# Performance work log

Measured on AMD Instinct MI355X. Metric: run time of the kernel, lower is better.

Reference implementation:

```python
import jax, jax.numpy as jnp
import numpy as np

# Qwen2 MoE MLP layer: top-k router -> token dispatch -> grouped SwiGLU MLP -> weighted combine.
S, B, H = 2048, 1, 1024      # seq, batch, hidden
E, K, F = 8, 2, 1408         # num_experts, top_k, moe_intermediate (fc1 emits 2*F for SwiGLU)

def setup_inputs() -> dict:
    key = jax.random.key(0)
    k1, k2, k3, k4 = jax.random.split(key, 4)
    return {
        "hidden_states": jax.random.normal(k1, (S, B, H), jnp.float32),
        "router_weight": jax.random.normal(k2, (H, E), jnp.float32) * 0.02,
        "w1": jax.random.normal(k3, (E, H, 2 * F), jnp.float32) * 0.02,  # grouped fc1 (gate|up)
        "w2": jax.random.normal(k4, (E, F, H), jnp.float32) * 0.02,      # grouped fc2
    }

def reference(hidden_states, router_weight, w1, w2):
    s, b, h = hidden_states.shape
    x = hidden_states.reshape(-1, h)                      # [T, H], T = S*B
    logits = x @ router_weight                            # [T, E]
    probs = jax.nn.softmax(logits, axis=-1)
    _, topk_idx = jax.lax.top_k(probs, K)                 # token -> top-k expert ids
    routing_map = jax.nn.one_hot(topk_idx, E, dtype=probs.dtype).sum(axis=1)  # [T, E] 0/1 mask
    local_probs = probs * routing_map                     # combine weights, zero off-topk
    # Grouped SwiGLU MLP. The torch module permutes tokens to expert groups and runs
    # grouped GEMMs; with static shapes the equivalent math is dense-per-expert with
    # the routing mask folded into the combine weights (identical output).
    y = jnp.einsum('th,ehf->tef', x, w1)                  # [T, E, 2F]
    y1, y2 = jnp.split(y, 2, axis=-1)
    g = jax.nn.silu(y1) * y2                              # swiglu, [T, E, F]
    o = jnp.einsum('tef,efh->teh', g, w2)                 # [T, E, H]
    out = jnp.einsum('teh,te->th', o, local_probs)        # unpermute + prob-weighted combine
    return out.reshape(s, b, h)
```

## Files before the change

### kernel.cpp

```cpp
#include <hip/hip_runtime.h>
#include <hip/hip_bf16.h>
#include <stdint.h>

#define T_TOK 2048
#define HD    1024
#define NE    8
#define FD    1408
#define F2D   2816

#define BM 128
#define BK 32
#define MAXMT 40
#define MAXSLOTS 5120
#define FC1_NT 22
#define FC2_NT 16
#define FC1_NWG (FC1_NT * MAXMT)
#define FC2_NWG (FC2_NT * MAXMT)
#define FC1_CHUNK 110
#define FC2_CHUNK 80

typedef __attribute__((ext_vector_type(8))) short bf16x8;
typedef __attribute__((ext_vector_type(4))) float f32x4;

__device__ __forceinline__ unsigned short f2bf(float f) {
  unsigned int u = __float_as_uint(f);
  u += 0x7FFFu + ((u >> 16) & 1u);
  return (unsigned short)(u >> 16);
}

#define GLL16(gp, lp) __builtin_amdgcn_global_load_lds( \
    (const __attribute__((address_space(1))) void*)(gp), \
    (__attribute__((address_space(3))) void*)(lp), 16, 0, 0)

__global__ __launch_bounds__(256) void k_router(
    const float* __restrict__ x, const float* __restrict__ rw,
    unsigned short* __restrict__ xbf, int* __restrict__ ctrl,
    int* __restrict__ tok_e, float* __restrict__ tok_p)
{
  const int lane = threadIdx.x & 63;
  const int t = blockIdx.x * 4 + (threadIdx.x >> 6);
  const float* xr = x + (size_t)t * HD;

  float part[8];
#pragma unroll
  for (int e = 0; e < 8; ++e) part[e] = 0.f;

#pragma unroll
  for (int i = 0; i < 16; ++i) {
    const int h = i * 64 + lane;
    const float xv = xr[h];
    xbf[(size_t)t * HD + h] = f2bf(xv);
    const float4* rwr = reinterpret_cast<const float4*>(rw + (size_t)h * 8);
    float4 a = rwr[0], b = rwr[1];
    part[0] += xv * a.x; part[1] += xv * a.y; part[2] += xv * a.z; part[3] += xv * a.w;
    part[4] += xv * b.x; part[5] += xv * b.y; part[6] += xv * b.z; part[7] += xv * b.w;
  }
#pragma unroll
  for (int e = 0; e < 8; ++e) {
    float v = part[e];
#pragma unroll
    for (int d = 32; d; d >>= 1) v += __shfl_xor(v, d, 64);
    part[e] = v;
  }
  float m = part[0];
#pragma unroll
  for (int e = 1; e < 8; ++e) m = fmaxf(m, part[e]);
  float p[8], s = 0.f;
#pragma unroll
  for (int e = 0; e < 8; ++e) { p[e] = __expf(part[e] - m); s += p[e]; }
  const float inv = 1.f / s;
#pragma unroll
  for (int e = 0; e < 8; ++e) p[e] *= inv;

  int e0 = 0; float p0 = p[0];
#pragma unroll
  for (int e = 1; e < 8; ++e) if (p[e] > p0) { p0 = p[e]; e0 = e; }
  int e1 = -1; float p1 = -1.f;
#pragma unroll
  for (int e = 0; e < 8; ++e) if (e != e0 && p[e] > p1) { p1 = p[e]; e1 = e; }

  if (lane == 0) {
    tok_e[t * 2 + 0] = e0; tok_e[t * 2 + 1] = e1;
    tok_p[t * 2 + 0] = p0; tok_p[t * 2 + 1] = p1;
    atomicAdd(&ctrl[e0], 1);
    atomicAdd(&ctrl[e1], 1);
  }
}

__global__ __launch_bounds__(256) void k_offsets(
    int* __restrict__ ctrl, int* __restrict__ stok, float* __restrict__ sp,
    int* __restrict__ widmt1, int* __restrict__ widmt2)
{
  __shared__ int soff[8], scnt[8], sFirst[8], sNmt[8], sTake[8];
  __shared__ int sSpill;
  if (threadIdx.x == 0) {
    int o = 0, nm = 0, spill = 0;
    for (int e = 0; e < 8; ++e) {
      ctrl[16 + e] = o; soff[e] = o; scnt[e] = ctrl[e];
      const int n = ctrl[e];
      const int nmt = (n + BM - 1) / BM;
      sFirst[e] = nm; sNmt[e] = nmt; sTake[e] = nmt < 5 ? nmt : 5;
      if (nmt > 5) spill = 1;
      for (int j = 0; j < nmt; ++j) { ctrl[24 + nm] = e; ctrl[64 + nm] = o + j * BM; ++nm; }
      o += nmt * BM;
    }
    for (int i = nm; i < MAXMT; ++i) ctrl[24 + i] = -1;
    sSpill = spill;
  }
  __syncthreads();
  for (int i = threadIdx.x; i < FC1_NWG; i += 256) {
    const int e = i / FC1_CHUNK, r = i % FC1_CHUNK;
    const int j = r / FC1_NT, n = r % FC1_NT;
    widmt1[i] = (j < sTake[e]) ? (sFirst[e] + j) * 32 + n : -1;
  }
  for (int i = threadIdx.x; i < FC2_NWG; i += 256) {
    const int e = i / FC2_CHUNK, r = i % FC2_CHUNK;
    const int j = r / FC2_NT, n = r % FC2_NT;
    widmt2[i] = (j < sTake[e]) ? (sFirst[e] + j) * 32 + n : -1;
  }
  __syncthreads();
  if (sSpill && threadIdx.x == 0) {
    int cur = 0;
    for (int e = 0; e < 8; ++e)
      for (int j = 5; j < sNmt[e]; ++j)
        for (int n = 0; n < FC1_NT; ++n) {
          while (widmt1[cur] != -1) ++cur;
          widmt1[cur] = (sFirst[e] + j) * 32 + n;
        }
    cur = 0;
    for (int e = 0; e < 8; ++e)
      for (int j = 5; j < sNmt[e]; ++j)
        for (int n = 0; n < FC2_NT; ++n) {
          while (widmt2[cur] != -1) ++cur;
          widmt2[cur] = (sFirst[e] + j) * 32 + n;
        }
  }
  for (int e = 0; e < 8; ++e) {
    const int n = scnt[e], o = soff[e];
    const int padEnd = (n + BM - 1) / BM * BM;
    for (int j = n + (int)threadIdx.x; j < padEnd; j += 256) {
      stok[o + j] = 0; sp[o + j] = 0.f;
    }
  }
}

__global__ __launch_bounds__(256) void k_scatter(
    int* __restrict__ ctrl, const int* __restrict__ tok_e,
    const float* __restrict__ tok_p, int* __restrict__ stok,
    float* __restrict__ sp, int* __restrict__ tslot)
{
  const int t = blockIdx.x * 256 + threadIdx.x;
#pragma unroll
  for (int k = 0; k < 2; ++k) {
    const int e = tok_e[t * 2 + k];
    const float pp = tok_p[t * 2 + k];
    const int pos = atomicAdd(&ctrl[8 + e], 1);
    const int slot = ctrl[16 + e] + pos;
    stok[slot] = t; sp[slot] = pp;
    tslot[t * 2 + k] = slot;
  }
}

__global__ __launch_bounds__(256) void k_transpose_cvt(
    const float* __restrict__ src, unsigned short* __restrict__ dst,
    int R, int C)
{
  const size_t zoff = (size_t)blockIdx.z * R * C;
  src += zoff; dst += zoff;
  const int r0 = blockIdx.y * 64, c0 = blockIdx.x * 64;
  __shared__ float tile[64][65];
  const int tr = threadIdx.x >> 4;
  const int tc = (threadIdx.x & 15) * 4;
#pragma unroll
  for (int p = 0; p < 4; ++p) {
    const int r = p * 16 + tr;
    float4 v = *reinterpret_cast<const float4*>(&src[(size_t)(r0 + r) * C + c0 + tc]);
    tile[r][tc + 0] = v.x; tile[r][tc + 1] = v.y;
    tile[r][tc + 2] = v.z; tile[r][tc + 3] = v.w;
  }
  __syncthreads();
#pragma unroll
  for (int p = 0; p < 4; ++p) {
    const int c = p * 16 + tr;
    ushort4 o;
    o.x = f2bf(tile[tc + 0][c]);
    o.y = f2bf(tile[tc + 1][c]);
    o.z = f2bf(tile[tc + 2][c]);
    o.w = f2bf(tile[tc + 3][c]);
    *reinterpret_cast<ushort4*>(&dst[(size_t)(c0 + c) * R + r0 + tc]) = o;
  }
}

__global__ __launch_bounds__(256) void k_fc1(
    const unsigned short* __restrict__ xbf,
    const unsigned short* __restrict__ w1t,
    const int* __restrict__ ctrl,
    const int* __restrict__ stok,
    const float* __restrict__ sp,
    const int* __restrict__ widmt1,
    unsigned short* __restrict__ g)
{
  const int bid = blockIdx.x;
  const int wid = (bid & 7) * FC1_CHUNK + (bid >> 3);
  const int packed = widmt1[wid];
  if (packed < 0) return;
  const int mt = packed >> 5;
  const int e = ctrl[24 + mt];
  const int rowbase = ctrl[64 + mt];
  const int n0 = (packed & 31) * 64;

  __shared__ unsigned short sA[3][BM * BK];
  __shared__ unsigned short sB1[3][64 * BK];
  __shared__ unsigned short sB2[3][64 * BK];

  const int tid = threadIdx.x;
  const int lane = tid & 63;
  const int wave = tid >> 6;
  const int wm = wave >> 1, wn = wave & 1;

  const int schunk = (lane & 3) ^ ((lane >> 3) & 3);
  const unsigned short* aSrc[2];
#pragma unroll
  for (int t4 = 0; t4 < 2; ++t4) {
    const int row = (t4 * 4 + wave) * 16 + (lane >> 2);
    const int tok = stok[rowbase + row];
    aSrc[t4] = xbf + (size_t)tok * HD + schunk * 8;
  }
  const int brow = wave * 16 + (lane >> 2);
  const unsigned short* b1Src = w1t + ((size_t)e * F2D + n0 + brow) * HD + schunk * 8;
  const unsigned short* b2Src = w1t + ((size_t)e * F2D + FD + n0 + brow) * HD + schunk * 8;

  const int c = lane >> 4;
  int aoff[4], boff[2];
#pragma unroll
  for (int m = 0; m < 4; ++m) {
    const int row = wm * 64 + m * 16 + (lane & 15);
    aoff[m] = row * 32 + ((c ^ ((row >> 1) & 3)) << 3);
  }
#pragma unroll
  for (int n = 0; n < 2; ++n) {
    const int row = wn * 32 + n * 16 + (lane & 15);
    boff[n] = row * 32 + ((c ^ ((row >> 1) & 3)) << 3);
  }

  const f32x4 zero = {0.f, 0.f, 0.f, 0.f};
  f32x4 acc1[4][2], acc2[4][2];
#pragma unroll
  for (int m = 0; m < 4; ++m)
#pragma unroll
    for (int n = 0; n < 2; ++n) { acc1[m][n] = zero; acc2[m][n] = zero; }

  auto STAGE = [&](int buf, int k0) {
#pragma unroll
    for (int t4 = 0; t4 < 2; ++t4)
      GLL16(aSrc[t4] + k0, &sA[buf][(t4 * 4 + wave) * 512]);
    GLL16(b1Src + k0, &sB1[buf][wave * 512]);
    GLL16(b2Src + k0, &sB2[buf][wave * 512]);
  };

  const int NSTEP = HD / BK;
  STAGE(0, 0);
  STAGE(1, BK);
  int bsel = 0;
  for (int t = 0; t < NSTEP; ++t) {
    if (t < NSTEP - 2) { asm volatile("s_waitcnt vmcnt(4)" ::: "memory"); }
    else               { asm volatile("s_waitcnt vmcnt(0)" ::: "memory"); }
    __builtin_amdgcn_s_barrier();
    __builtin_amdgcn_sched_barrier(0);
    if (t + 2 < NSTEP) {
      int bnext = bsel + 2; if (bnext >= 3) bnext -= 3;
      STAGE(bnext, (t + 2) * BK);
    }
    bf16x8 af[4], b1f[2], b2f[2];
#pragma unroll
    for (int m = 0; m < 4; ++m)
      af[m] = *(const bf16x8*)&sA[bsel][aoff[m]];
#pragma unroll
    for (int n = 0; n < 2; ++n) {
      b1f[n] = *(const bf16x8*)&sB1[bsel][boff[n]];
      b2f[n] = *(const bf16x8*)&sB2[bsel][boff[n]];
    }
    asm volatile("s_waitcnt lgkmcnt(0)" ::: "memory");
    __builtin_amdgcn_sched_barrier(0);
    __builtin_amdgcn_s_setprio(1);
#pragma unroll
    for (int m = 0; m < 4; ++m)
#pragma unroll
      for (int n = 0; n < 2; ++n) {
        acc1[m][n] = __builtin_amdgcn_mfma_f32_16x16x32_bf16(af[m], b1f[n], acc1[m][n], 0, 0, 0);
        acc2[m][n] = __builtin_amdgcn_mfma_f32_16x16x32_bf16(af[m], b2f[n], acc2[m][n], 0, 0, 0);
      }
    __builtin_amdgcn_s_setprio(0);
    bsel = bsel + 1 == 3 ? 0 : bsel + 1;
  }

  float prv[4][4];
#pragma unroll
  for (int m = 0; m < 4; ++m)
#pragma unroll
    for (int r = 0; r < 4; ++r)
      prv[m][r] = sp[rowbase + wm * 64 + m * 16 + (lane >> 4) * 4 + r];

#pragma unroll
  for (int m = 0; m < 4; ++m) {
    const int rb = rowbase + wm * 64 + m * 16 + (lane >> 4) * 4;
#pragma unroll
    for (int n = 0; n < 2; ++n) {
      const int col = n0 + wn * 32 + n * 16 + (lane & 15);
#pragma unroll
      for (int r = 0; r < 4; ++r) {
        const float y1 = acc1[m][n][r];
        const float y2 = acc2[m][n][r];
        const float gv = y1 / (1.f + __expf(-y1)) * y2 * prv[m][r];
        g[(size_t)(rb + r) * FD + col] = f2bf(gv);
      }
    }
  }
}

__global__ __launch_bounds__(256) void k_fc2(
    const unsigned short* __restrict__ g,
    const unsigned short* __restrict__ w2t,
    const int* __restrict__ ctrl,
    const int* __restrict__ widmt2,
    float* __restrict__ o)
{
  const int bid = blockIdx.x;
  const int wid = (bid & 7) * FC2_CHUNK + (bid >> 3);
  const int packed = widmt2[wid];
  if (packed < 0) return;
  const int mt = packed >> 5;
  const int e = ctrl[24 + mt];
  const int rowbase = ctrl[64 + mt];
  const int n0 = (packed & 31) * 64;

  __shared__ unsigned short sA[3][BM * BK];
  __shared__ unsigned short sB[3][64 * BK];

  const int tid = threadIdx.x;
  const int lane = tid & 63;
  const int wave = tid >> 6;
  const int wm = wave >> 1, wn = wave & 1;

  const int schunk = (lane & 3) ^ ((lane >> 3) & 3);
  const unsigned short* aSrc[2];
#pragma unroll
  for (int t4 = 0; t4 < 2; ++t4) {
    const int row = (t4 * 4 + wave) * 16 + (lane >> 2);
    aSrc[t4] = g + (size_t)(rowbase + row) * FD + schunk * 8;
  }
  const int brow = wave * 16 + (lane >> 2);
  const unsigned short* bSrc = w2t + ((size_t)e * HD + n0 + brow) * FD + schunk * 8;

  const int c = lane >> 4;
  int aoff[4], boff[2];
#pragma unroll
  for (int m = 0; m < 4; ++m) {
    const int row = wm * 64 + m * 16 + (lane & 15);
    aoff[m] = row * 32 + ((c ^ ((row >> 1) & 3)) << 3);
  }
#pragma unroll
  for (int n = 0; n < 2; ++n) {
    const int row = wn * 32 + n * 16 + (lane & 15);
    boff[n] = row * 32 + ((c ^ ((row >> 1) & 3)) << 3);
  }

  const f32x4 zero = {0.f, 0.f, 0.f, 0.f};
  f32x4 acc[4][2];
#pragma unroll
  for (int m = 0; m < 4; ++m)
#pragma unroll
    for (int n = 0; n < 2; ++n) acc[m][n] = zero;

  auto STAGE = [&](int buf, int k0) {
#pragma unroll
    for (int t4 = 0; t4 < 2; ++t4)
      GLL16(aSrc[t4] + k0, &sA[buf][(t4 * 4 + wave) * 512]);
    GLL16(bSrc + k0, &sB[buf][wave * 512]);
  };

  const int NSTEP = FD / BK;
  STAGE(0, 0);
  STAGE(1, BK);
  int bsel = 0;
  for (int t = 0; t < NSTEP; ++t) {
    if (t < NSTEP - 2) { asm volatile("s_waitcnt vmcnt(3)" ::: "memory"); }
    else               { asm volatile("s_waitcnt vmcnt(0)" ::: "memory"); }
    __builtin_amdgcn_s_barrier();
    __builtin_amdgcn_sched_barrier(0);
    if (t + 2 < NSTEP) {
      int bnext = bsel + 2; if (bnext >= 3) bnext -= 3;
      STAGE(bnext, (t + 2) * BK);
    }
    bf16x8 af[4], bf[2];
#pragma unroll
    for (int m = 0; m < 4; ++m)
      af[m] = *(const bf16x8*)&sA[bsel][aoff[m]];
#pragma unroll
    for (int n = 0; n < 2; ++n)
      bf[n] = *(const bf16x8*)&sB[bsel][boff[n]];
    asm volatile("s_waitcnt lgkmcnt(0)" ::: "memory");
    __builtin_amdgcn_sched_barrier(0);
    __builtin_amdgcn_s_setprio(1);
#pragma unroll
    for (int m = 0; m < 4; ++m)
#pragma unroll
      for (int n = 0; n < 2; ++n)
        acc[m][n] = __builtin_amdgcn_mfma_f32_16x16x32_bf16(af[m], bf[n], acc[m][n], 0, 0, 0);
    __builtin_amdgcn_s_setprio(0);
    bsel = bsel + 1 == 3 ? 0 : bsel + 1;
  }

#pragma unroll
  for (int m = 0; m < 4; ++m) {
    const int rb = rowbase + wm * 64 + m * 16 + (lane >> 4) * 4;
#pragma unroll
    for (int n = 0; n < 2; ++n) {
      const int col = n0 + wn * 32 + n * 16 + (lane & 15);
#pragma unroll
      for (int r = 0; r < 4; ++r)
        o[(size_t)(rb + r) * HD + col] = acc[m][n][r];
    }
  }
}

__global__ __launch_bounds__(256) void k_combine(
    const float* __restrict__ o, const int* __restrict__ tslot,
    float* __restrict__ out)
{
  const int t = blockIdx.x;
  const int c4 = threadIdx.x;
  const int sA = tslot[t * 2], sB = tslot[t * 2 + 1];
  const float4 a = reinterpret_cast<const float4*>(o)[(size_t)sA * 256 + c4];
  const float4 b = reinterpret_cast<const float4*>(o)[(size_t)sB * 256 + c4];
  float4 r;
  r.x = a.x + b.x; r.y = a.y + b.y; r.z = a.z + b.z; r.w = a.w + b.w;
  reinterpret_cast<float4*>(out)[(size_t)t * 256 + c4] = r;
}

extern "C" void kernel_launch(void* const* d_in, const int* in_sizes, int n_in,
                              void* d_out, int out_size, void* d_ws, size_t ws_size,
                              hipStream_t stream)
{
  const float* x  = (const float*)d_in[0];
  const float* rw = (const float*)d_in[1];
  const float* w1 = (const float*)d_in[2];
  const float* w2 = (const float*)d_in[3];
  float* out = (float*)d_out;
  char* ws = (char*)d_ws;

  int*   ctrl   = (int*)(ws + 0);
  int*   tok_e  = (int*)(ws + 1024);
  float* tok_p  = (float*)(ws + 17408);
  int*   stok   = (int*)(ws + 33792);
  float* sp     = (float*)(ws + 54272);
  int*   tslot  = (int*)(ws + 74752);
  int*   widmt1 = (int*)(ws + 91136);
  int*   widmt2 = (int*)(ws + 94656);
  unsigned short* xbf = (unsigned short*)(ws + 97280);
  unsigned short* w1t = (unsigned short*)(ws + 4291584);
  unsigned short* w2t = (unsigned short*)(ws + 50428928);
  unsigned short* g   = (unsigned short*)(ws + 73497600);
  float* o = (float*)(ws + 4291584);

  hipMemsetAsync(ws, 0, 1024, stream);

  k_router<<<T_TOK / 4, 256, 0, stream>>>(x, rw, xbf, ctrl, tok_e, tok_p);
  k_transpose_cvt<<<dim3(F2D / 64, HD / 64, NE), 256, 0, stream>>>(w1, w1t, HD, F2D);
  k_transpose_cvt<<<dim3(HD / 64, FD / 64, NE), 256, 0, stream>>>(w2, w2t, FD, HD);
  k_offsets<<<1, 256, 0, stream>>>(ctrl, stok, sp, widmt1, widmt2);
  k_scatter<<<T_TOK / 256, 256, 0, stream>>>(ctrl, tok_e, tok_p, stok, sp, tslot);
  k_fc1<<<FC1_NWG, 256, 0, stream>>>(xbf, w1t, ctrl, stok, sp, widmt1, g);
  k_fc2<<<FC2_NWG, 256, 0, stream>>>(g, w2t, ctrl, widmt2, o);
  k_combine<<<T_TOK, 256, 0, stream>>>(o, tslot, out);
}
```

Baseline: 208.2 us.

## Fuse weight transpose and bf16 conversion into expert GEMM B-tile loads

```diff
diff --git a/kernel.cpp b/kernel.cpp
--- a/kernel.cpp
+++ b/kernel.cpp
@@ -161,39 +161,9 @@
   }
 }
 
-__global__ __launch_bounds__(256) void k_transpose_cvt(
-    const float* __restrict__ src, unsigned short* __restrict__ dst,
-    int R, int C)
-{
-  const size_t zoff = (size_t)blockIdx.z * R * C;
-  src += zoff; dst += zoff;
-  const int r0 = blockIdx.y * 64, c0 = blockIdx.x * 64;
-  __shared__ float tile[64][65];
-  const int tr = threadIdx.x >> 4;
-  const int tc = (threadIdx.x & 15) * 4;
-#pragma unroll
-  for (int p = 0; p < 4; ++p) {
-    const int r = p * 16 + tr;
-    float4 v = *reinterpret_cast<const float4*>(&src[(size_t)(r0 + r) * C + c0 + tc]);
-    tile[r][tc + 0] = v.x; tile[r][tc + 1] = v.y;
-    tile[r][tc + 2] = v.z; tile[r][tc + 3] = v.w;
-  }
-  __syncthreads();
-#pragma unroll
-  for (int p = 0; p < 4; ++p) {
-    const int c = p * 16 + tr;
-    ushort4 o;
-    o.x = f2bf(tile[tc + 0][c]);
-    o.y = f2bf(tile[tc + 1][c]);
-    o.z = f2bf(tile[tc + 2][c]);
-    o.w = f2bf(tile[tc + 3][c]);
-    *reinterpret_cast<ushort4*>(&dst[(size_t)(c0 + c) * R + r0 + tc]) = o;
-  }
-}
-
 __global__ __launch_bounds__(256) void k_fc1(
     const unsigned short* __restrict__ xbf,
-    const unsigned short* __restrict__ w1t,
+    const float* __restrict__ w1,
     const int* __restrict__ ctrl,
     const int* __restrict__ stok,
     const float* __restrict__ sp,
@@ -226,9 +196,32 @@
     const int tok = stok[rowbase + row];
     aSrc[t4] = xbf + (size_t)tok * HD + schunk * 8;
   }
-  const int brow = wave * 16 + (lane >> 2);
-  const unsigned short* b1Src = w1t + ((size_t)e * F2D + n0 + brow) * HD + schunk * 8;
-  const unsigned short* b2Src = w1t + ((size_t)e * F2D + FD + n0 + brow) * HD + schunk * 8;
+
+  const float* bbase = w1 + (size_t)e * HD * F2D
+                     + ((wave & 2) ? (size_t)(FD + n0 + lane) : (size_t)(n0 + lane));
+  float breg[16];
+  auto BLOAD = [&](int k0) {
+    const float* p = bbase + (size_t)(k0 + (wave & 1) * 16) * F2D;
+#pragma unroll
+    for (int j = 0; j < 16; ++j) breg[j] = p[(size_t)j * F2D];
+  };
+  auto BWRITE = [&](int buf) {
+    unsigned short* dst = (wave & 2) ? sB2[buf] : sB1[buf];
+    const int xr = (lane >> 1) & 3;
+#pragma unroll
+    for (int cc = 0; cc < 2; ++cc) {
+      const int cw = (wave & 1) * 2 + cc;
+      bf16x8 v;
+#pragma unroll
+      for (int jj = 0; jj < 8; ++jj) v[jj] = (short)f2bf(breg[cc * 8 + jj]);
+      *(bf16x8*)&dst[lane * 32 + ((cw ^ xr) << 3)] = v;
+    }
+  };
+  auto ASTAGE = [&](int buf, int k0) {
+#pragma unroll
+    for (int t4 = 0; t4 < 2; ++t4)
+      GLL16(aSrc[t4] + k0, &sA[buf][(t4 * 4 + wave) * 512]);
+  };
 
   const int c = lane >> 4;
   int aoff[4], boff[2];
@@ -250,26 +243,33 @@
 #pragma unroll
     for (int n = 0; n < 2; ++n) { acc1[m][n] = zero; acc2[m][n] = zero; }
 
-  auto STAGE = [&](int buf, int k0) {
-#pragma unroll
-    for (int t4 = 0; t4 < 2; ++t4)
-      GLL16(aSrc[t4] + k0, &sA[buf][(t4 * 4 + wave) * 512]);
-    GLL16(b1Src + k0, &sB1[buf][wave * 512]);
-    GLL16(b2Src + k0, &sB2[buf][wave * 512]);
-  };
-
   const int NSTEP = HD / BK;
-  STAGE(0, 0);
-  STAGE(1, BK);
+  BLOAD(0);
+  __builtin_amdgcn_sched_barrier(0);
+  ASTAGE(0, 0);
+  __builtin_amdgcn_sched_barrier(0);
+  asm volatile("s_waitcnt vmcnt(2)" ::: "memory");
+  BWRITE(0);
+  BLOAD(BK);
+  __builtin_amdgcn_sched_barrier(0);
+  ASTAGE(1, BK);
+  __builtin_amdgcn_sched_barrier(0);
+  asm volatile("s_waitcnt lgkmcnt(0)" ::: "memory");
+
   int bsel = 0;
   for (int t = 0; t < NSTEP; ++t) {
-    if (t < NSTEP - 2) { asm volatile("s_waitcnt vmcnt(4)" ::: "memory"); }
+    if (t < NSTEP - 2) { asm volatile("s_waitcnt vmcnt(2)" ::: "memory"); }
     else               { asm volatile("s_waitcnt vmcnt(0)" ::: "memory"); }
     __builtin_amdgcn_s_barrier();
     __builtin_amdgcn_sched_barrier(0);
+    int bnext = bsel + 1; if (bnext >= 3) bnext -= 3;
+    int bn2 = bsel + 2; if (bn2 >= 3) bn2 -= 3;
+    if (t + 1 < NSTEP) BWRITE(bnext);
     if (t + 2 < NSTEP) {
-      int bnext = bsel + 2; if (bnext >= 3) bnext -= 3;
-      STAGE(bnext, (t + 2) * BK);
+      BLOAD((t + 2) * BK);
+      __builtin_amdgcn_sched_barrier(0);
+      ASTAGE(bn2, (t + 2) * BK);
+      __builtin_amdgcn_sched_barrier(0);
     }
     bf16x8 af[4], b1f[2], b2f[2];
 #pragma unroll
@@ -291,7 +291,7 @@
         acc2[m][n] = __builtin_amdgcn_mfma_f32_16x16x32_bf16(af[m], b2f[n], acc2[m][n], 0, 0, 0);
       }
     __builtin_amdgcn_s_setprio(0);
-    bsel = bsel + 1 == 3 ? 0 : bsel + 1;
+    bsel = bnext;
   }
 
   float prv[4][4];
@@ -320,7 +320,7 @@
 
 __global__ __launch_bounds__(256) void k_fc2(
     const unsigned short* __restrict__ g,
-    const unsigned short* __restrict__ w2t,
+    const float* __restrict__ w2,
     const int* __restrict__ ctrl,
     const int* __restrict__ widmt2,
     float* __restrict__ o)
@@ -349,8 +349,26 @@
     const int row = (t4 * 4 + wave) * 16 + (lane >> 2);
     aSrc[t4] = g + (size_t)(rowbase + row) * FD + schunk * 8;
   }
-  const int brow = wave * 16 + (lane >> 2);
-  const unsigned short* bSrc = w2t + ((size_t)e * HD + n0 + brow) * FD + schunk * 8;
+
+  const float* bbase = w2 + (size_t)e * FD * HD + n0 + lane;
+  float breg[8];
+  auto BLOAD = [&](int k0) {
+    const float* p = bbase + (size_t)(k0 + wave * 8) * HD;
+#pragma unroll
+    for (int j = 0; j < 8; ++j) breg[j] = p[(size_t)j * HD];
+  };
+  auto BWRITE = [&](int buf) {
+    const int xr = (lane >> 1) & 3;
+    bf16x8 v;
+#pragma unroll
+    for (int jj = 0; jj < 8; ++jj) v[jj] = (short)f2bf(breg[jj]);
+    *(bf16x8*)&sB[buf][lane * 32 + ((wave ^ xr) << 3)] = v;
+  };
+  auto ASTAGE = [&](int buf, int k0) {
+#pragma unroll
+    for (int t4 = 0; t4 < 2; ++t4)
+      GLL16(aSrc[t4] + k0, &sA[buf][(t4 * 4 + wave) * 512]);
+  };
 
   const int c = lane >> 4;
   int aoff[4], boff[2];
@@ -372,25 +390,33 @@
 #pragma unroll
     for (int n = 0; n < 2; ++n) acc[m][n] = zero;
 
-  auto STAGE = [&](int buf, int k0) {
-#pragma unroll
-    for (int t4 = 0; t4 < 2; ++t4)
-      GLL16(aSrc[t4] + k0, &sA[buf][(t4 * 4 + wave) * 512]);
-    GLL16(bSrc + k0, &sB[buf][wave * 512]);
-  };
-
   const int NSTEP = FD / BK;
-  STAGE(0, 0);
-  STAGE(1, BK);
+  BLOAD(0);
+  __builtin_amdgcn_sched_barrier(0);
+  ASTAGE(0, 0);
+  __builtin_amdgcn_sched_barrier(0);
+  asm volatile("s_waitcnt vmcnt(2)" ::: "memory");
+  BWRITE(0);
+  BLOAD(BK);
+  __builtin_amdgcn_sched_barrier(0);
+  ASTAGE(1, BK);
+  __builtin_amdgcn_sched_barrier(0);
+  asm volatile("s_waitcnt lgkmcnt(0)" ::: "memory");
+
   int bsel = 0;
   for (int t = 0; t < NSTEP; ++t) {
-    if (t < NSTEP - 2) { asm volatile("s_waitcnt vmcnt(3)" ::: "memory"); }
+    if (t < NSTEP - 2) { asm volatile("s_waitcnt vmcnt(2)" ::: "memory"); }
     else               { asm volatile("s_waitcnt vmcnt(0)" ::: "memory"); }
     __builtin_amdgcn_s_barrier();
     __builtin_amdgcn_sched_barrier(0);
+    int bnext = bsel + 1; if (bnext >= 3) bnext -= 3;
+    int bn2 = bsel + 2; if (bn2 >= 3) bn2 -= 3;
+    if (t + 1 < NSTEP) BWRITE(bnext);
     if (t + 2 < NSTEP) {
-      int bnext = bsel + 2; if (bnext >= 3) bnext -= 3;
-      STAGE(bnext, (t + 2) * BK);
+      BLOAD((t + 2) * BK);
+      __builtin_amdgcn_sched_barrier(0);
+      ASTAGE(bn2, (t + 2) * BK);
+      __builtin_amdgcn_sched_barrier(0);
     }
     bf16x8 af[4], bf[2];
 #pragma unroll
@@ -408,7 +434,7 @@
       for (int n = 0; n < 2; ++n)
         acc[m][n] = __builtin_amdgcn_mfma_f32_16x16x32_bf16(af[m], bf[n], acc[m][n], 0, 0, 0);
     __builtin_amdgcn_s_setprio(0);
-    bsel = bsel + 1 == 3 ? 0 : bsel + 1;
+    bsel = bnext;
   }
 
 #pragma unroll
@@ -458,19 +484,15 @@
   int*   widmt1 = (int*)(ws + 91136);
   int*   widmt2 = (int*)(ws + 94656);
   unsigned short* xbf = (unsigned short*)(ws + 97280);
-  unsigned short* w1t = (unsigned short*)(ws + 4291584);
-  unsigned short* w2t = (unsigned short*)(ws + 50428928);
-  unsigned short* g   = (unsigned short*)(ws + 73497600);
-  float* o = (float*)(ws + 4291584);
+  unsigned short* g   = (unsigned short*)(ws + 4291584);
+  float*          o   = (float*)(ws + 18709504);
 
   hipMemsetAsync(ws, 0, 1024, stream);
 
   k_router<<<T_TOK / 4, 256, 0, stream>>>(x, rw, xbf, ctrl, tok_e, tok_p);
-  k_transpose_cvt<<<dim3(F2D / 64, HD / 64, NE), 256, 0, stream>>>(w1, w1t, HD, F2D);
-  k_transpose_cvt<<<dim3(HD / 64, FD / 64, NE), 256, 0, stream>>>(w2, w2t, FD, HD);
   k_offsets<<<1, 256, 0, stream>>>(ctrl, stok, sp, widmt1, widmt2);
   k_scatter<<<T_TOK / 256, 256, 0, stream>>>(ctrl, tok_e, tok_p, stok, sp, tslot);
-  k_fc1<<<FC1_NWG, 256, 0, stream>>>(xbf, w1t, ctrl, stok, sp, widmt1, g);
-  k_fc2<<<FC2_NWG, 256, 0, stream>>>(g, w2t, ctrl, widmt2, o);
+  k_fc1<<<FC1_NWG, 256, 0, stream>>>(xbf, w1, ctrl, stok, sp, widmt1, g);
+  k_fc2<<<FC2_NWG, 256, 0, stream>>>(g, w2, ctrl, widmt2, o);
   k_combine<<<T_TOK, 256, 0, stream>>>(o, tslot, out);
 }
```

After: 213.9 us. 1.03x slower.
